# Performance work log

Hardware: AMD Instinct MI355X
Metric: run time of the kernel (lower is better)

The kernel has to match this reference:

```python
import jax, jax.numpy as jnp
import numpy as np

BLOCK_CONFIGS = [[4, 64, 64], [64, 128, 128], [128, 256, 256], [256, 512]]
KNN_K = 16
PN, PL, PM = 5, 3, 3          # kernel polynomial degrees (N, L, M)
BASIS = PN * PL * PM          # 45 monomial basis functions
NUM_LAYERS = 4
N_POINTS = 32768


def get_reduction_schedule(n_input, n_target, num_layers):
    # geometric point-count reduction from n_input down to n_target
    r = (n_target / n_input) ** (1.0 / num_layers)
    return [max(n_target, int(round(n_input * r ** (i + 1)))) for i in range(num_layers)]


def knn_idx(qpos, spos, k):
    # squared distances via the |q|^2 + |s|^2 - 2 q.s identity (avoids (q,s,3) temp)
    d = jnp.sum(qpos * qpos, 1)[:, None] + jnp.sum(spos * spos, 1)[None, :] - 2.0 * (qpos @ spos.T)
    _, idx = jax.lax.top_k(-d, k)  # (q, k) nearest-neighbor indices
    return idx


def poly_basis(r):
    # monomial basis x^i y^j z^k, i<PN, j<PL, k<PM -> (q, k, BASIS)
    x, y, z = r[..., 0], r[..., 1], r[..., 2]
    px = x[..., None] ** jnp.arange(PN)
    py = y[..., None] ** jnp.arange(PL)
    pz = z[..., None] ** jnp.arange(PM)
    phi = px[..., :, None, None] * py[..., None, :, None] * pz[..., None, None, :]
    return phi.reshape(r.shape[:-1] + (BASIS,))


def dcconv(qpos, spos, sfeat, k, W, b, use_pca=True):
    # KNN gather -> normalized relative coords -> (PCA align) -> polynomial kernel conv
    idx = knn_idx(qpos, spos, k)
    r = spos[idx] - qpos[:, None, :]                         # (q, k, 3)
    scale = jnp.max(jnp.sqrt(jnp.sum(r * r, -1)), axis=-1, keepdims=True)
    r = r / (scale[..., None] + 1e-8)
    if use_pca:
        cov = jnp.einsum('qki,qkj->qij', r, r) / k           # (q, 3, 3)
        _, vecs = jnp.linalg.eigh(cov)
        vecs = jax.lax.stop_gradient(vecs)                   # PCA frame treated as constant
        r = jnp.einsum('qki,qij->qkj', r, vecs)
    phi = poly_basis(r)                                       # (q, k, B)
    nf = sfeat[idx]                                           # (q, k, Cin)
    t = jnp.einsum('qkb,qkc->qbc', phi, nf) / k               # neighbor reduce (mean)
    return jnp.einsum('qbc,bco->qo', t, W) + b


def _forward(position_matrix, channel_matrix, ws, bs, ps, head_w, head_b):
    sched = get_reduction_schedule(position_matrix.shape[0], 1, NUM_LAYERS)
    pos, feat = position_matrix, channel_matrix
    li = 0
    for bi, cfg in enumerate(BLOCK_CONFIGS):
        n_sel = sched[bi]
        qpos = pos[:n_sel]                                    # selector: first n_sel centers
        res = feat[:n_sel] @ ps[bi]                           # residual projection
        x, src_pos = feat, pos
        for _ in range(len(cfg) - 1):
            k = min(KNN_K, src_pos.shape[0])
            x = jax.nn.relu(dcconv(qpos, src_pos, x, k, ws[li], bs[li]))
            li += 1
            src_pos = qpos                                    # subsequent layers: self-conv on reduced set
        feat = jax.nn.relu(x + res)
        pos = qpos
    if feat.shape[0] > 1:
        feat = feat.mean(0, keepdims=True)
    return (feat @ head_w + head_b)[0]                        # (out_channels,) = (1,)


def setup_inputs():
    key = jax.random.key(0)
    ks = jax.random.split(key, 32)
    inp = {}
    inp['position_matrix'] = jax.random.normal(ks[0], (N_POINTS, 3), dtype=jnp.float32)
    inp['channel_matrix'] = jax.random.normal(ks[1], (N_POINTS, 4), dtype=jnp.float32)
    i, li = 2, 1
    for cfg in BLOCK_CONFIGS:
        for cin, cout in zip(cfg[:-1], cfg[1:]):
            inp[f'w{li}'] = jax.random.normal(ks[i], (BASIS, cin, cout), dtype=jnp.float32) * 0.05
            inp[f'b{li}'] = jnp.zeros((cout,), dtype=jnp.float32)
            i += 1
            li += 1
    for bi, cfg in enumerate(BLOCK_CONFIGS):
        inp[f'p{bi + 1}'] = jax.random.normal(ks[i], (cfg[0], cfg[-1]), dtype=jnp.float32) * 0.05
        i += 1
    inp['head_w'] = jax.random.normal(ks[i], (BLOCK_CONFIGS[-1][-1], 1), dtype=jnp.float32) * 0.05
    inp['head_b'] = jnp.zeros((1,), dtype=jnp.float32)
    return inp


def reference(position_matrix, channel_matrix, w1, b1, w2, b2, w3, b3, w4, b4, w5, b5, w6, b6, w7, b7,
              p1, p2, p3, p4, head_w, head_b):
    ws = [w1, w2, w3, w4, w5, w6, w7]
    bs = [b1, b2, b3, b4, b5, b6, b7]
    ps = [p1, p2, p3, p4]
    return _forward(position_matrix, channel_matrix, ws, bs, ps, head_w, head_b)
```

## Files before the change

### kernel.cpp

```cpp
#include <hip/hip_runtime.h>
#include <math.h>

#pragma clang fp contract(off)

__device__ __forceinline__ float f_sign(float a, float b) {
    return (b >= 0.0f) ? fabsf(a) : -fabsf(a);
}

__device__ float slapy2(float x, float y) {
    float xa = fabsf(x), ya = fabsf(y);
    float w = fmaxf(xa, ya), z = fminf(xa, ya);
    if (z == 0.0f) return w;
    float t = z / w;
    return w * sqrtf(1.0f + t * t);
}

__device__ void slartg(float f, float g, float &cs, float &sn, float &r) {
    if (g == 0.0f) { cs = 1.0f; sn = 0.0f; r = f; }
    else if (f == 0.0f) { cs = 0.0f; sn = f_sign(1.0f, g); r = fabsf(g); }
    else {
        float d = sqrtf(f * f + g * g);
        float p = 1.0f / d;
        cs = fabsf(f) * p;
        sn = g * f_sign(p, f);
        r = f_sign(d, f);
    }
}

__device__ void slaev2(float a, float b, float c,
                       float &rt1, float &rt2, float &cs1, float &sn1) {
    float sm = a + c, df = a - c, adf = fabsf(df), tb = b + b, ab = fabsf(tb);
    float acmx, acmn;
    if (fabsf(a) > fabsf(c)) { acmx = a; acmn = c; } else { acmx = c; acmn = a; }
    float rt;
    if (adf > ab) { float t = ab / adf; rt = adf * sqrtf(1.0f + t * t); }
    else if (adf < ab) { float t = adf / ab; rt = ab * sqrtf(1.0f + t * t); }
    else rt = ab * sqrtf(2.0f);
    int sgn1;
    if (sm < 0.0f) { rt1 = 0.5f * (sm - rt); sgn1 = -1; rt2 = (acmx / rt1) * acmn - (b / rt1) * b; }
    else if (sm > 0.0f) { rt1 = 0.5f * (sm + rt); sgn1 = 1; rt2 = (acmx / rt1) * acmn - (b / rt1) * b; }
    else { rt1 = 0.5f * rt; rt2 = -0.5f * rt; sgn1 = 1; }
    float cs; int sgn2;
    if (df >= 0.0f) { cs = df + rt; sgn2 = 1; } else { cs = df - rt; sgn2 = -1; }
    float acs = fabsf(cs);
    if (acs > ab) { float ct = -tb / cs; sn1 = 1.0f / sqrtf(1.0f + ct * ct); cs1 = ct * sn1; }
    else {
        if (ab == 0.0f) { cs1 = 1.0f; sn1 = 0.0f; }
        else { float tn = -cs / tb; cs1 = 1.0f / sqrtf(1.0f + tn * tn); sn1 = tn * cs1; }
    }
    if (sgn1 == sgn2) { float tn = cs1; cs1 = -sn1; sn1 = tn; }
}

__device__ void ssteqr3(float *d, float *e, float z[3][3]) {
    const int n = 3;
    const float eps = 5.9604644775390625e-08f;
    const float eps2 = eps * eps;
    const float safmin = 1.1754943508222875e-38f;
    for (int i = 0; i < 3; ++i)
        for (int j = 0; j < 3; ++j)
            z[i][j] = (i == j) ? 1.0f : 0.0f;
    const int nmaxit = n * 30;
    int jtot = 0;
    int l1 = 1;
    int l, m, lend;
    float p, g, r, c, s, f, b, rt1, rt2;
    float wc[2], wsn[2];

L10:
    if (l1 > n) goto L160;
    if (l1 > 1) e[l1 - 2] = 0.0f;
    if (l1 <= n - 1) {
        for (m = l1; m <= n - 1; ++m) {
            float tst = fabsf(e[m - 1]);
            if (tst == 0.0f) goto L30;
            if (tst <= (sqrtf(fabsf(d[m - 1])) * sqrtf(fabsf(d[m]))) * eps) {
                e[m - 1] = 0.0f;
                goto L30;
            }
        }
    }
    m = n;
L30:
    l = l1;
    lend = m;
    l1 = m + 1;
    if (lend == l) goto L10;
    {
        float anorm = 0.0f;
        for (int i = l; i <= lend; ++i) anorm = fmaxf(anorm, fabsf(d[i - 1]));
        for (int i = l; i <= lend - 1; ++i) anorm = fmaxf(anorm, fabsf(e[i - 1]));
        if (anorm == 0.0f) goto L10;
    }
    if (fabsf(d[lend - 1]) < fabsf(d[l - 1])) { int t = lend; lend = l; l = t; }

    if (lend > l) {
L40:
        if (l != lend) {
            bool found = false;
            for (m = l; m <= lend - 1; ++m) {
                float tst = e[m - 1] * e[m - 1];
                if (tst <= (eps2 * fabsf(d[m - 1])) * fabsf(d[m]) + safmin) { found = true; break; }
            }
            if (!found) m = lend;
        } else m = lend;
        if (m < lend) e[m - 1] = 0.0f;
        p = d[l - 1];
        if (m == l) goto L80;
        if (m == l + 1) {
            slaev2(d[l - 1], e[l - 1], d[l], rt1, rt2, c, s);
            for (int i = 0; i < n; ++i) {
                float tmp = z[i][l];
                z[i][l]     = c * tmp - s * z[i][l - 1];
                z[i][l - 1] = s * tmp + c * z[i][l - 1];
            }
            d[l - 1] = rt1; d[l] = rt2; e[l - 1] = 0.0f;
            l += 2;
            if (l <= lend) goto L40;
            goto L140;
        }
        if (jtot == nmaxit) goto L140;
        ++jtot;
        g = (d[l] - p) / (2.0f * e[l - 1]);
        r = slapy2(g, 1.0f);
        g = (d[m - 1] - p) + e[l - 1] / (g + f_sign(r, g));
        s = 1.0f; c = 1.0f; p = 0.0f;
        for (int i = m - 1; i >= l; --i) {
            f = s * e[i - 1];
            b = c * e[i - 1];
            slartg(g, f, c, s, r);
            if (i != m - 1) e[i] = r;
            g = d[i] - p;
            r = (d[i - 1] - g) * s + (2.0f * c) * b;
            p = s * r;
            d[i] = g + p;
            g = c * r - b;
            wc[i - 1] = c;
            wsn[i - 1] = -s;
        }
        for (int jj = m - 1; jj >= l; --jj) {
            float ct = wc[jj - 1], st = wsn[jj - 1];
            for (int i = 0; i < n; ++i) {
                float tmp = z[i][jj];
                z[i][jj]     = ct * tmp - st * z[i][jj - 1];
                z[i][jj - 1] = st * tmp + ct * z[i][jj - 1];
            }
        }
        d[l - 1] -= p;
        e[l - 1] = g;
        goto L40;
L80:
        d[l - 1] = p;
        ++l;
        if (l <= lend) goto L40;
        goto L140;
    } else {
L90:
        if (l != lend) {
            bool found = false;
            for (m = l; m >= lend + 1; --m) {
                float tst = e[m - 2] * e[m - 2];
                if (tst <= (eps2 * fabsf(d[m - 1])) * fabsf(d[m - 2]) + safmin) { found = true; break; }
            }
            if (!found) m = lend;
        } else m = lend;
        if (m > lend) e[m - 2] = 0.0f;
        p = d[l - 1];
        if (m == l) goto L130;
        if (m == l - 1) {
            slaev2(d[l - 2], e[l - 2], d[l - 1], rt1, rt2, c, s);
            for (int i = 0; i < n; ++i) {
                float tmp = z[i][l - 1];
                z[i][l - 1] = c * tmp - s * z[i][l - 2];
                z[i][l - 2] = s * tmp + c * z[i][l - 2];
            }
            d[l - 2] = rt1; d[l - 1] = rt2; e[l - 2] = 0.0f;
            l -= 2;
            if (l >= lend) goto L90;
            goto L140;
        }
        if (jtot == nmaxit) goto L140;
        ++jtot;
        g = (d[l - 2] - p) / (2.0f * e[l - 2]);
        r = slapy2(g, 1.0f);
        g = (d[m - 1] - p) + e[l - 2] / (g + f_sign(r, g));
        s = 1.0f; c = 1.0f; p = 0.0f;
        for (int i = m; i <= l - 1; ++i) {
            f = s * e[i - 1];
            b = c * e[i - 1];
            slartg(g, f, c, s, r);
            if (i != m) e[i - 2] = r;
            g = d[i - 1] - p;
            r = (d[i] - g) * s + (2.0f * c) * b;
            p = s * r;
            d[i - 1] = g + p;
            g = c * r - b;
            wc[i - 1] = c;
            wsn[i - 1] = s;
        }
        for (int jj = m; jj <= l - 1; ++jj) {
            float ct = wc[jj - 1], st = wsn[jj - 1];
            for (int i = 0; i < n; ++i) {
                float tmp = z[i][jj];
                z[i][jj]     = ct * tmp - st * z[i][jj - 1];
                z[i][jj - 1] = st * tmp + ct * z[i][jj - 1];
            }
        }
        d[l - 1] -= p;
        e[l - 2] = g;
        goto L90;
L130:
        d[l - 1] = p;
        --l;
        if (l >= lend) goto L90;
        goto L140;
    }
L140:
    if (jtot < nmaxit) goto L10;
L160:
    for (int ii = 2; ii <= n; ++ii) {
        int i = ii - 1, kk = i;
        float pp = d[i - 1];
        for (int j = ii; j <= n; ++j)
            if (d[j - 1] < pp) { kk = j; pp = d[j - 1]; }
        if (kk != i) {
            d[kk - 1] = d[i - 1];
            d[i - 1] = pp;
            for (int row = 0; row < n; ++row) {
                float t2 = z[row][i - 1];
                z[row][i - 1] = z[row][kk - 1];
                z[row][kk - 1] = t2;
            }
        }
    }
}

__device__ void ssyevd3(float a11, float a21, float a31,
                        float a22, float a32, float a33, float V[3][3]) {
    float tau1, v2, e1;
    float alpha = a21;
    float xnorm = fabsf(a31);
    if (xnorm == 0.0f) {
        tau1 = 0.0f; v2 = 0.0f; e1 = a21;
    } else {
        float beta = -f_sign(slapy2(alpha, xnorm), alpha);
        tau1 = (beta - alpha) / beta;
        float t = 1.0f / (alpha - beta);
        v2 = a31 * t;
        e1 = beta;
        float w1 = tau1 * a22;
        float w2 = tau1 * a32;
        float temp2 = a32 * v2;
        w1 = w1 + tau1 * temp2;
        float temp1 = tau1 * v2;
        w2 = w2 + temp1 * a33;
        float dot = w1;
        dot = dot + w2 * v2;
        float alpha2 = (-0.5f * tau1) * dot;
        w1 = w1 + alpha2;
        w2 = w2 + alpha2 * v2;
        a22 = (a22 - w1) - w1;
        a32 = (a32 - v2 * w1) - w2;
        a33 = (a33 - v2 * w2) - w2 * v2;
    }
    float d[3] = { a11, a22, a33 };
    float e[2] = { e1, a32 };
    float z[3][3];
    ssteqr3(d, e, z);
    for (int j = 0; j < 3; ++j) {
        float wj = z[1][j];
        wj = wj + z[2][j] * v2;
        float temp = (-tau1) * wj;
        V[0][j] = z[0][j];
        V[1][j] = z[1][j] + temp;
        V[2][j] = z[2][j] + v2 * temp;
    }
}

__device__ void geom_body(const float *__restrict__ posf, const int *__restrict__ ord,
                          int q, int k, float *__restrict__ rrot) {
    float qx = posf[3 * q], qy = posf[3 * q + 1], qz = posf[3 * q + 2];
    float rx[16], ry[16], rz[16], nrm[16];
    for (int j = 0; j < k; ++j) {
        int s = ord[j];
        rx[j] = posf[3 * s] - qx;
        ry[j] = posf[3 * s + 1] - qy;
        rz[j] = posf[3 * s + 2] - qz;
        float t = rx[j] * rx[j];
        t = t + ry[j] * ry[j];
        t = t + rz[j] * rz[j];
        nrm[j] = sqrtf(t);
    }
    float scale = nrm[0];
    for (int j = 1; j < k; ++j) scale = fmaxf(scale, nrm[j]);
    float sc = scale + 1e-8f;
    for (int j = 0; j < k; ++j) {
        rx[j] = rx[j] / sc;
        ry[j] = ry[j] / sc;
        rz[j] = rz[j] / sc;
    }
    float c00 = 0.f, c01 = 0.f, c02 = 0.f, c11 = 0.f, c12 = 0.f, c22 = 0.f;
    for (int j = 0; j < k; ++j) {
        c00 = c00 + rx[j] * rx[j];
        c01 = c01 + rx[j] * ry[j];
        c02 = c02 + rx[j] * rz[j];
        c11 = c11 + ry[j] * ry[j];
        c12 = c12 + ry[j] * rz[j];
        c22 = c22 + rz[j] * rz[j];
    }
    float fk = (float)k;
    c00 = c00 / fk; c01 = c01 / fk; c02 = c02 / fk;
    c11 = c11 / fk; c12 = c12 / fk; c22 = c22 / fk;
    float V[3][3];
    ssyevd3(c00, c01, c02, c11, c12, c22, V);
    for (int j = 0; j < k; ++j) {
        for (int col = 0; col < 3; ++col) {
            float a = rx[j] * V[0][col];
            a = a + ry[j] * V[1][col];
            a = a + rz[j] * V[2][col];
            rrot[q * 48 + j * 3 + col] = a;
        }
    }
}


__global__ void prep_kernel(const float *__restrict__ posf, float4 *__restrict__ pos4) {
    int i = blockIdx.x * 256 + threadIdx.x;
    if (i >= 32768) return;
    float x = posf[3 * i], y = posf[3 * i + 1], z = posf[3 * i + 2];
    float t = x * x;
    t = t + y * y;
    t = t + z * z;
    pos4[i] = make_float4(x, y, z, t);
}

__device__ __forceinline__ void insert16(float d, int jbase, int lane,
                                         float &ld, int &li, float &kth) {
    unsigned long long mask = __ballot(d < kth);
    while (mask) {
        int src = __ffsll(mask) - 1;
        mask &= mask - 1;
        float dv = __int_as_float(__builtin_amdgcn_readlane(__float_as_int(d), src));
        int jv = jbase + src;
        if (dv < kth) {
            unsigned long long lm = __ballot((lane < 16) && (ld <= dv));
            int p2 = __popcll(lm);
            float sd = __int_as_float(__builtin_amdgcn_update_dpp(
                0, __float_as_int(ld), 0x111, 0xf, 0xf, true));
            int si = __builtin_amdgcn_update_dpp(0, li, 0x111, 0xf, 0xf, true);
            if (lane < 16) {
                if (lane == p2) { ld = dv; li = jv; }
                else if (lane > p2) { ld = sd; li = si; }
            }
            kth = __int_as_float(__builtin_amdgcn_readlane(__float_as_int(ld), 15));
        }
    }
}

__device__ __forceinline__ void sort64_init(float d, int jbase, int lane,
                                            float &ld, int &li, float &kth) {
    float v = d;
    int vi = jbase + lane;
#pragma unroll
    for (int k2 = 2; k2 <= 64; k2 <<= 1) {
#pragma unroll
        for (int j2 = k2 >> 1; j2 > 0; j2 >>= 1) {
            float ov = __shfl_xor(v, j2);
            int oi = __shfl_xor(vi, j2);
            bool oless = (ov < v) || (ov == v && oi < vi);
            bool dir = ((lane & k2) == 0);
            bool keepmin = (((lane & j2) == 0) == dir);
            bool take = keepmin ? oless : !oless;
            if (take) { v = ov; vi = oi; }
        }
    }
    if (lane < 16) { ld = v; li = vi; }
    kth = __int_as_float(__builtin_amdgcn_readlane(__float_as_int(v), 15));
}

__global__ __launch_bounds__(256) void knng16_kernel(
    const float4 *__restrict__ pos4, const float *__restrict__ posf,
    int S, int *__restrict__ idx_out, float *__restrict__ rrot) {
    __shared__ float md[64];
    __shared__ int mi[64];
    __shared__ int ord[16];
    int q = blockIdx.x;
    int tid = threadIdx.x;
    int lane = tid & 63;
    int w = tid >> 6;
    float4 qp = pos4[q];
    const float FINF = 3.0e38f;
    float ld = FINF;
    int li = 0x7fffffff;
    float kth = FINF;
    int base = w * 256;
    float4 c0, c1, c2, c3;
    bool have = (base + 256 <= S);
    bool first = true;
    if (have) {
        c0 = pos4[base + lane];
        c1 = pos4[base + 64 + lane];
        c2 = pos4[base + 128 + lane];
        c3 = pos4[base + 192 + lane];
    }
    while (have) {
        int nbase = base + 1024;
        bool nhave = (nbase + 256 <= S);
        float4 n0 = c0, n1 = c1, n2 = c2, n3 = c3;
        if (nhave) {
            n0 = pos4[nbase + lane];
            n1 = pos4[nbase + 64 + lane];
            n2 = pos4[nbase + 128 + lane];
            n3 = pos4[nbase + 192 + lane];
        }
        float m0 = fmaf(qp.x, c0.x, 0.0f);
        m0 = fmaf(qp.y, c0.y, m0);
        m0 = fmaf(qp.z, c0.z, m0);
        float d0 = (qp.w + c0.w) - 2.0f * m0;
        float m1 = fmaf(qp.x, c1.x, 0.0f);
        m1 = fmaf(qp.y, c1.y, m1);
        m1 = fmaf(qp.z, c1.z, m1);
        float d1 = (qp.w + c1.w) - 2.0f * m1;
        float m2 = fmaf(qp.x, c2.x, 0.0f);
        m2 = fmaf(qp.y, c2.y, m2);
        m2 = fmaf(qp.z, c2.z, m2);
        float d2 = (qp.w + c2.w) - 2.0f * m2;
        float m3 = fmaf(qp.x, c3.x, 0.0f);
        m3 = fmaf(qp.y, c3.y, m3);
        m3 = fmaf(qp.z, c3.z, m3);
        float d3 = (qp.w + c3.w) - 2.0f * m3;
        if (first) {
            sort64_init(d0, base, lane, ld, li, kth);
            first = false;
        } else {
            insert16(d0, base, lane, ld, li, kth);
        }
        insert16(d1, base + 64, lane, ld, li, kth);
        insert16(d2, base + 128, lane, ld, li, kth);
        insert16(d3, base + 192, lane, ld, li, kth);
        c0 = n0; c1 = n1; c2 = n2; c3 = n3;
        base = nbase;
        have = nhave;
    }
    if (base < S) {
#pragma unroll
        for (int k2 = 0; k2 < 4; ++k2) {
            int j = base + k2 * 64 + lane;
            float dd = FINF;
            if (j < S) {
                float4 p = pos4[j];
                float m = fmaf(qp.x, p.x, 0.0f);
                m = fmaf(qp.y, p.y, m);
                m = fmaf(qp.z, p.z, m);
                dd = (qp.w + p.w) - 2.0f * m;
            }
            insert16(dd, base + k2 * 64, lane, ld, li, kth);
        }
    }
    if (lane < 16) { md[w * 16 + lane] = ld; mi[w * 16 + lane] = li; }
    __syncthreads();
    if (w == 0) {
        int l16 = lane & 15;
        int srcA = (lane >> 5) * 32 + ((lane & 16) ? (16 + (15 - l16)) : l16);
        float v = md[srcA];
        int vi = mi[srcA];
        for (int off = 16; off > 0; off >>= 1) {
            float ov = __shfl_xor(v, off);
            int oi = __shfl_xor(vi, off);
            bool oless = (ov < v) || (ov == v && oi < vi);
            bool take = (lane & off) ? (!oless) : oless;
            if (take) { v = ov; vi = oi; }
        }
        int src2 = (lane < 16) ? lane : (63 - lane);
        float v2 = __shfl(v, src2);
        int vi2 = __shfl(vi, src2);
        for (int off = 16; off > 0; off >>= 1) {
            float ov = __shfl_xor(v2, off);
            int oi = __shfl_xor(vi2, off);
            bool oless = (ov < v2) || (ov == v2 && oi < vi2);
            bool take = (lane & off) ? (!oless) : oless;
            if (take) { v2 = ov; vi2 = oi; }
        }
        if (lane < 16) {
            idx_out[q * 16 + lane] = vi2;
            ord[lane] = vi2;
        }
        if (lane == 0) geom_body(posf, ord, q, 16, rrot);
    }
}

__global__ __launch_bounds__(64) void knngs_kernel(
    const float4 *__restrict__ pos4, const float *__restrict__ posf,
    int S, int k, int *__restrict__ idx_out, float *__restrict__ rrot) {
    __shared__ int ord[16];
    int q = blockIdx.x;
    int lane = threadIdx.x;
    float4 qp = pos4[q];
    const float FINF = 3.0e38f;
    float dist = FINF;
    if (lane < S) {
        float4 p = pos4[lane];
        float m = fmaf(qp.x, p.x, 0.0f);
        m = fmaf(qp.y, p.y, m);
        m = fmaf(qp.z, p.z, m);
        dist = (qp.w + p.w) - 2.0f * m;
    }
    bool used = false;
    for (int r = 0; r < k; ++r) {
        float v = used ? FINF : dist;
        int vid = (used || lane >= S) ? 0x7fffffff : lane;
        for (int off = 32; off > 0; off >>= 1) {
            float ov = __shfl_down(v, off);
            int oid = __shfl_down(vid, off);
            if (ov < v || (ov == v && oid < vid)) { v = ov; vid = oid; }
        }
        vid = __shfl(vid, 0);
        if (lane == 0) { idx_out[q * k + r] = vid; ord[r] = vid; }
        if (lane == vid) used = true;
    }
    if (lane == 0) geom_body(posf, ord, q, k, rrot);
}

__device__ __forceinline__ void compute_phi(const float *rrot, int q, int tid,
                                            double phi[45]) {
    double x = (double)rrot[q * 48 + tid * 3 + 0];
    double y = (double)rrot[q * 48 + tid * 3 + 1];
    double z = (double)rrot[q * 48 + tid * 3 + 2];
    double px[5], py[3], pz[3];
    px[0] = 1.0; px[1] = x; px[2] = x * x; px[3] = px[2] * x; px[4] = px[3] * x;
    py[0] = 1.0; py[1] = y; py[2] = y * y;
    pz[0] = 1.0; pz[1] = z; pz[2] = z * z;
#pragma unroll
    for (int n2 = 0; n2 < 5; ++n2)
#pragma unroll
        for (int l2 = 0; l2 < 3; ++l2)
#pragma unroll
            for (int m2 = 0; m2 < 3; ++m2)
                phi[n2 * 9 + l2 * 3 + m2] = (px[n2] * py[l2]) * pz[m2];
}

__global__ __launch_bounds__(256) void feat_kernel(
    const float *__restrict__ rrot, const int *__restrict__ idx, int k,
    const double *__restrict__ fin64, const float *__restrict__ fin32, int C,
    const float *__restrict__ W, const float *__restrict__ bias, int O,
    double *__restrict__ fout) {
    __shared__ double phi_sh[16][45];
    __shared__ int idx_sh[16];
    __shared__ double red_sh[256];
    extern __shared__ double dyn[];
    double *nf = dyn;
    double *t = dyn + 16 * C;
    int q = blockIdx.x;
    int tid = threadIdx.x;
    int OT = O < 256 ? O : 256;
    int nseg = 256 / OT;
    int o = tid % OT;
    int seg = tid / OT;
    int cseg = C / nseg;
    int c0 = seg * cseg, c1 = c0 + cseg;
    if (tid < k) {
        idx_sh[tid] = idx[q * k + tid];
        double phi[45];
        compute_phi(rrot, q, tid, phi);
#pragma unroll
        for (int b2 = 0; b2 < 45; ++b2) phi_sh[tid][b2] = phi[b2];
    }
    __syncthreads();
    for (int e2 = tid; e2 < k * C; e2 += 256) {
        int j = e2 / C, cc = e2 - j * C;
        size_t src = (size_t)idx_sh[j] * C + cc;
        nf[j * C + cc] = fin32 ? (double)fin32[src] : fin64[src];
    }
    __syncthreads();
    double accp = 0.0;
    for (int ch = 0; ch < 45; ch += 9) {
        for (int e2 = tid; e2 < 9 * C; e2 += 256) {
            int b2 = e2 / C, cc = e2 - b2 * C;
            double a2 = 0.0;
            for (int j = 0; j < k; ++j) a2 = fma(phi_sh[j][ch + b2], nf[j * C + cc], a2);
            t[e2] = a2 / (double)k;
        }
        __syncthreads();
        double a0 = 0.0, a1 = 0.0;
        for (int b2 = 0; b2 < 9; ++b2) {
            const float *wp = W + (size_t)(ch + b2) * C * O + o;
            const double *tp = t + b2 * C;
            int cc = c0;
            for (; cc + 2 <= c1; cc += 2) {
                a0 = fma(tp[cc],     (double)wp[(size_t)cc * O], a0);
                a1 = fma(tp[cc + 1], (double)wp[(size_t)(cc + 1) * O], a1);
            }
            for (; cc < c1; ++cc) a0 = fma(tp[cc], (double)wp[(size_t)cc * O], a0);
        }
        accp += a0 + a1;
        __syncthreads();
    }
    red_sh[tid] = accp;
    __syncthreads();
    if (tid < OT) {
        double v = 0.0;
        for (int s2 = 0; s2 < nseg; ++s2) v += red_sh[tid + s2 * OT];
        v += (double)bias[tid];
        fout[(size_t)q * O + tid] = v > 0.0 ? v : 0.0;
    }
}

__global__ __launch_bounds__(256) void feat64_kernel(
    const float *__restrict__ rrot, const int *__restrict__ idx,
    const double *__restrict__ fin, const float *__restrict__ W,
    const float *__restrict__ bias, int Q, double *__restrict__ fout) {
    __shared__ double phi_sh[2][16][45];
    __shared__ int idx_sh[2][16];
    __shared__ double nf[2][16][64];
    __shared__ double t[2][9][64];
    __shared__ double red[16][64];
    int q0 = blockIdx.x * 2;
    int nq = (Q - q0) < 2 ? (Q - q0) : 2;
    int tid = threadIdx.x;
    int tx = tid & 15;
    int seg = tid >> 4;
    int o0 = tx * 4;
    int cbase = seg * 4;
    if (tid < 32) {
        int qi = tid >> 4, j = tid & 15;
        int qq = q0 + (qi < nq ? qi : 0);
        idx_sh[qi][j] = idx[qq * 16 + j];
        double phi[45];
        compute_phi(rrot, qq, j, phi);
#pragma unroll
        for (int b2 = 0; b2 < 45; ++b2) phi_sh[qi][j][b2] = phi[b2];
    }
    __syncthreads();
    for (int e2 = tid; e2 < 2 * 16 * 64; e2 += 256) {
        int qi = e2 >> 10, j = (e2 >> 6) & 15, cc = e2 & 63;
        nf[qi][j][cc] = fin[(size_t)idx_sh[qi][j] * 64 + cc];
    }
    __syncthreads();
    double acc[2][4] = {{0.0, 0.0, 0.0, 0.0}, {0.0, 0.0, 0.0, 0.0}};
    for (int ch = 0; ch < 45; ch += 9) {
        for (int e2 = tid; e2 < 2 * 9 * 64; e2 += 256) {
            int qi = e2 / 576, rem = e2 - qi * 576;
            int b2 = rem >> 6, cc = rem & 63;
            double a2 = 0.0;
#pragma unroll
            for (int j = 0; j < 16; ++j) a2 = fma(phi_sh[qi][j][ch + b2], nf[qi][j][cc], a2);
            t[qi][b2][cc] = a2 * 0.0625;
        }
        __syncthreads();
#pragma unroll
        for (int b2 = 0; b2 < 9; ++b2) {
            const float *wrow = W + ((size_t)(ch + b2) * 64 + cbase) * 64 + o0;
#pragma unroll
            for (int i = 0; i < 4; ++i) {
                float4 wv = *(const float4 *)(wrow + (size_t)i * 64);
                double w0 = (double)wv.x, w1 = (double)wv.y;
                double w2 = (double)wv.z, w3 = (double)wv.w;
                double tv0 = t[0][b2][cbase + i];
                double tv1 = t[1][b2][cbase + i];
                acc[0][0] = fma(tv0, w0, acc[0][0]);
                acc[0][1] = fma(tv0, w1, acc[0][1]);
                acc[0][2] = fma(tv0, w2, acc[0][2]);
                acc[0][3] = fma(tv0, w3, acc[0][3]);
                acc[1][0] = fma(tv1, w0, acc[1][0]);
                acc[1][1] = fma(tv1, w1, acc[1][1]);
                acc[1][2] = fma(tv1, w2, acc[1][2]);
                acc[1][3] = fma(tv1, w3, acc[1][3]);
            }
        }
        __syncthreads();
    }
    for (int qi = 0; qi < nq; ++qi) {
        red[seg][o0 + 0] = acc[qi][0];
        red[seg][o0 + 1] = acc[qi][1];
        red[seg][o0 + 2] = acc[qi][2];
        red[seg][o0 + 3] = acc[qi][3];
        __syncthreads();
        if (tid < 64) {
            double v = 0.0;
#pragma unroll
            for (int s2 = 0; s2 < 16; ++s2) v += red[s2][tid];
            v += (double)bias[tid];
            fout[(size_t)(q0 + qi) * 64 + tid] = v > 0.0 ? v : 0.0;
        }
        __syncthreads();
    }
}

__global__ __launch_bounds__(256) void t_kernel(
    const float *__restrict__ rrot, const int *__restrict__ idx, int k,
    const double *__restrict__ fin, int C, int q0, double *__restrict__ tbuf,
    double *__restrict__ fout, int O) {
    __shared__ double phi_sh[16][45];
    __shared__ int idx_sh[16];
    extern __shared__ double nf[];
    int q = q0 + blockIdx.x;
    int bch = blockIdx.y * 9;
    int tid = threadIdx.x;
    if (blockIdx.y == 0) {
        for (int i = tid; i < O; i += 256) fout[(size_t)q * O + i] = 0.0;
    }
    if (tid < k) {
        idx_sh[tid] = idx[q * k + tid];
        double phi[45];
        compute_phi(rrot, q, tid, phi);
#pragma unroll
        for (int b2 = 0; b2 < 45; ++b2) phi_sh[tid][b2] = phi[b2];
    }
    __syncthreads();
    for (int e2 = tid; e2 < k * C; e2 += 256) {
        int j = e2 / C, cc = e2 - j * C;
        nf[j * C + cc] = fin[(size_t)idx_sh[j] * C + cc];
    }
    __syncthreads();
    int K = 45 * C;
    for (int e2 = tid; e2 < 9 * C; e2 += 256) {
        int b2 = bch + e2 / C, cc = e2 % C;
        double a2 = 0.0;
        for (int j = 0; j < k; ++j) a2 = fma(phi_sh[j][b2], nf[j * C + cc], a2);
        tbuf[(size_t)blockIdx.x * K + b2 * C + cc] = a2 / (double)k;
    }
}

__global__ __launch_bounds__(256) void gemm_kernel(
    const double *__restrict__ tbuf, const float *__restrict__ W,
    int K, int O, int q0, int q1, int kchunk, double *__restrict__ acc) {
    int OT = O < 256 ? O : 256;
    int qpb = 256 / OT;
    int tid = threadIdx.x;
    int o = blockIdx.x * OT + (tid % OT);
    int q = q0 + blockIdx.y * qpb + tid / OT;
    if (q >= q1) return;
    int k0 = blockIdx.z * kchunk;
    if (k0 >= K) return;
    int kend = min(k0 + kchunk, K);
    const double *tp = tbuf + (size_t)(q - q0) * K;
    const float *wp = W + (size_t)k0 * O + o;
    double a0 = 0.0, a1 = 0.0, a2 = 0.0, a3 = 0.0;
    double a4 = 0.0, a5 = 0.0, a6 = 0.0, a7 = 0.0;
    int kk = k0;
    for (; kk + 8 <= kend; kk += 8) {
        double2 t01 = *(const double2 *)(tp + kk);
        double2 t23 = *(const double2 *)(tp + kk + 2);
        double2 t45 = *(const double2 *)(tp + kk + 4);
        double2 t67 = *(const double2 *)(tp + kk + 6);
        float w0 = wp[0];
        float w1 = wp[(size_t)O];
        float w2 = wp[2 * (size_t)O];
        float w3 = wp[3 * (size_t)O];
        float w4 = wp[4 * (size_t)O];
        float w5 = wp[5 * (size_t)O];
        float w6 = wp[6 * (size_t)O];
        float w7 = wp[7 * (size_t)O];
        a0 = fma(t01.x, (double)w0, a0);
        a1 = fma(t01.y, (double)w1, a1);
        a2 = fma(t23.x, (double)w2, a2);
        a3 = fma(t23.y, (double)w3, a3);
        a4 = fma(t45.x, (double)w4, a4);
        a5 = fma(t45.y, (double)w5, a5);
        a6 = fma(t67.x, (double)w6, a6);
        a7 = fma(t67.y, (double)w7, a7);
        wp += 8 * (size_t)O;
    }
    for (; kk < kend; ++kk) {
        a0 = fma(tp[kk], (double)wp[0], a0);
        wp += (size_t)O;
    }
    double s = ((a0 + a1) + (a2 + a3)) + ((a4 + a5) + (a6 + a7));
    atomicAdd(&acc[(size_t)q * O + o], s);
}

__global__ void finalize_kernel(const float *__restrict__ bias,
                                int Q, int O, double *__restrict__ fout) {
    int i = blockIdx.x * 256 + threadIdx.x;
    if (i >= Q * O) return;
    int o = i % O;
    double v = fout[i] + (double)bias[o];
    fout[i] = v > 0.0 ? v : 0.0;
}

__global__ void resid0_kernel(const float *__restrict__ chanf, const float *__restrict__ p,
                              const double *__restrict__ x, double *__restrict__ fout) {
    int i = blockIdx.x * 256 + threadIdx.x;
    if (i >= 2435 * 64) return;
    int q = i >> 6, o = i & 63;
    const float *f = chanf + 4 * q;
    float c = fmaf(f[0], p[o], 0.0f);
    c = fmaf(f[1], p[64 + o], c);
    c = fmaf(f[2], p[128 + o], c);
    c = fmaf(f[3], p[192 + o], c);
    double v = x[i] + (double)c;
    fout[i] = v > 0.0 ? v : 0.0;
}

__global__ void resid64f_kernel(const float *__restrict__ bias,
                                const double *__restrict__ acc,
                                const double *__restrict__ fin, int Cin,
                                const float *__restrict__ p,
                                int Q, int Cout, double *__restrict__ fout) {
    int i = blockIdx.x * blockDim.x + threadIdx.x;
    if (i >= Q * Cout) return;
    int q = i / Cout, o = i - q * Cout;
    double v = acc[i] + (double)bias[o];
    double x = v > 0.0 ? v : 0.0;
    double a = 0.0;
    for (int c = 0; c < Cin; ++c) a = fma(fin[q * Cin + c], (double)p[c * Cout + o], a);
    double r = x + a;
    fout[i] = r > 0.0 ? r : 0.0;
}

__global__ void head_kernel(const double *__restrict__ feat, const float *__restrict__ hw,
                            const float *__restrict__ hb, float *__restrict__ out) {
    if (threadIdx.x == 0 && blockIdx.x == 0) {
        double acc = 0.0;
        for (int c = 0; c < 512; ++c) acc = fma(feat[c], (double)hw[c], acc);
        out[0] = (float)(acc + (double)hb[0]);
    }
}


extern "C" void kernel_launch(void *const *d_in, const int *in_sizes, int n_in,
                              void *d_out, int out_size, void *d_ws, size_t ws_size,
                              hipStream_t stream) {
    (void)in_sizes; (void)n_in; (void)out_size;

    const float *posf = (const float *)d_in[0];
    const float *chanf = (const float *)d_in[1];
    const float *W[8], *B[8];
    for (int li = 1; li <= 7; ++li) {
        W[li] = (const float *)d_in[2 + 2 * (li - 1)];
        B[li] = (const float *)d_in[3 + 2 * (li - 1)];
    }
    const float *P[5];
    for (int bi = 1; bi <= 4; ++bi) P[bi] = (const float *)d_in[15 + bi];
    const float *hw = (const float *)d_in[20];
    const float *hb = (const float *)d_in[21];

    char *wsb = (char *)d_ws;
    double *B1   = (double *)(wsb + 0);
    double *B2   = (double *)(wsb + 1246720);
    double *B3   = (double *)(wsb + 2493440);
    float *rrot  = (float *)(wsb + 3740160);
    int *idx     = (int *)(wsb + 4207680);
    float4 *pos4 = (float4 *)(wsb + 4363520);
    double *tbuf = (double *)(wsb + 4887808);
    if (ws_size < 9082112) return;

    prep_kernel<<<128, 256, 0, stream>>>(posf, pos4);

    auto knng = [&](int Q, int S, int k) {
        if (S <= 64)
            knngs_kernel<<<Q, 64, 0, stream>>>(pos4, posf, S, k, idx, rrot);
        else
            knng16_kernel<<<Q, 256, 0, stream>>>(pos4, posf, S, idx, rrot);
    };

    auto conv = [&](int Q, int S, int k, const double *fin64, const float *fin32, int C,
                    const float *w, const float *bias, int O, double *fout) {
        knng(Q, S, k);
        size_t dyn = (size_t)(16 + 9) * C * sizeof(double);
        feat_kernel<<<Q, 256, dyn, stream>>>(rrot, idx, k, fin64, fin32, C, w, bias, O, fout);
    };

    auto conv64 = [&](int Q, int S, const double *fin, const float *w,
                      const float *bias, double *fout) {
        knng(Q, S, 16);
        feat64_kernel<<<(Q + 1) / 2, 256, 0, stream>>>(rrot, idx, fin, w, bias, Q, fout);
    };

    auto conv2 = [&](int Q, int S, int k, const double *fin, int C,
                     const float *w, const float *bias, int O, double *fout,
                     int ksplit, bool do_finalize, bool skip_knn) {
        if (!skip_knn) knng(Q, S, k);
        int K = 45 * C;
        int qc = 4194304 / (K * 8);
        if (qc > Q) qc = Q;
        int OT = O < 256 ? O : 256;
        int qpb = 256 / OT;
        int kchunk = (((K + ksplit - 1) / ksplit) + 7) & ~7;
        for (int q0 = 0; q0 < Q; q0 += qc) {
            int qn = min(qc, Q - q0);
            dim3 gt(qn, 5);
            t_kernel<<<gt, 256, (size_t)16 * C * sizeof(double), stream>>>(
                rrot, idx, k, fin, C, q0, tbuf, fout, O);
            dim3 g(O / OT, (qn + qpb - 1) / qpb, ksplit);
            gemm_kernel<<<g, 256, 0, stream>>>(tbuf, w, K, O, q0, q0 + qn, kchunk, fout);
        }
        if (do_finalize)
            finalize_kernel<<<(Q * O + 255) / 256, 256, 0, stream>>>(bias, Q, O, fout);
    };

    conv(2435, 32768, 16, nullptr, chanf, 4, W[1], B[1], 64, B1);
    conv64(2435, 2435, B1, W[2], B[2], B2);
    resid0_kernel<<<(2435 * 64 + 255) / 256, 256, 0, stream>>>(chanf, P[1], B2, B3);
    conv2(181, 2435, 16, B3, 64, W[3], B[3], 128, B1, 24, true, true);
    conv2(181, 181, 16, B1, 128, W[4], B[4], 128, B2, 24, false, false);
    resid64f_kernel<<<(181 * 128 + 255) / 256, 256, 0, stream>>>(
        B[4], B2, B3, 64, P[2], 181, 128, B1);
    conv2(13, 181, 16, B1, 128, W[5], B[5], 256, B2, 96, true, true);
    conv2(13, 13, 13, B2, 256, W[6], B[6], 256, B3, 96, false, false);
    resid64f_kernel<<<(13 * 256 + 255) / 256, 256, 0, stream>>>(
        B[6], B3, B1, 128, P[3], 13, 256, B2);
    conv2(1, 13, 13, B2, 256, W[7], B[7], 512, B1, 256, false, true);
    resid64f_kernel<<<(1 * 512 + 255) / 256, 256, 0, stream>>>(
        B[7], B1, B2, 256, P[4], 1, 512, B3);

    head_kernel<<<1, 64, 0, stream>>>(B3, hw, hb, (float *)d_out);
}
```

Measured before the change: 804.6 us.

## Split large KNN scans across blocks and skip insertion when no candidate beats kth

The KNN scan is factored into a helper. Each 256-candidate chunk now skips the bitonic insert16 work when no lane's minimum distance beats the current 16th-best (checked with a wave ballot). For source sets of 8192 points or more, the scan is split across 4 blocks per query, each writing a partial top-16 to workspace, and a separate merge kernel combines them and runs the geometry step. This adds parallelism for the first layer with many points, at the cost of an extra launch and global traffic for the partial results. The partial buffers reuse the tbuf workspace region.

```diff
diff --git a/kernel.cpp b/kernel.cpp
--- a/kernel.cpp
+++ b/kernel.cpp
@@ -377,24 +377,13 @@
     kth = __int_as_float(__builtin_amdgcn_readlane(__float_as_int(v), 15));
 }
 
-__global__ __launch_bounds__(256) void knng16_kernel(
-    const float4 *__restrict__ pos4, const float *__restrict__ posf,
-    int S, int *__restrict__ idx_out, float *__restrict__ rrot) {
-    __shared__ float md[64];
-    __shared__ int mi[64];
-    __shared__ int ord[16];
-    int q = blockIdx.x;
-    int tid = threadIdx.x;
-    int lane = tid & 63;
-    int w = tid >> 6;
-    float4 qp = pos4[q];
+__device__ __forceinline__ void scan_range(
+    const float4 *__restrict__ pos4, float4 qp, int start, int end, int lane,
+    float &ld, int &li, float &kth) {
     const float FINF = 3.0e38f;
-    float ld = FINF;
-    int li = 0x7fffffff;
-    float kth = FINF;
-    int base = w * 256;
+    int base = start;
     float4 c0, c1, c2, c3;
-    bool have = (base + 256 <= S);
+    bool have = (base + 256 <= end);
     bool first = true;
     if (have) {
         c0 = pos4[base + lane];
@@ -404,7 +393,7 @@
     }
     while (have) {
         int nbase = base + 1024;
-        bool nhave = (nbase + 256 <= S);
+        bool nhave = (nbase + 256 <= end);
         float4 n0 = c0, n1 = c1, n2 = c2, n3 = c3;
         if (nhave) {
             n0 = pos4[nbase + lane];
@@ -428,25 +417,28 @@
         m3 = fmaf(qp.y, c3.y, m3);
         m3 = fmaf(qp.z, c3.z, m3);
         float d3 = (qp.w + c3.w) - 2.0f * m3;
-        if (first) {
-            sort64_init(d0, base, lane, ld, li, kth);
-            first = false;
-        } else {
-            insert16(d0, base, lane, ld, li, kth);
-        }
-        insert16(d1, base + 64, lane, ld, li, kth);
-        insert16(d2, base + 128, lane, ld, li, kth);
-        insert16(d3, base + 192, lane, ld, li, kth);
+        float dmin = fminf(fminf(d0, d1), fminf(d2, d3));
+        if (first || __ballot(dmin < kth)) {
+            if (first) {
+                sort64_init(d0, base, lane, ld, li, kth);
+                first = false;
+            } else {
+                insert16(d0, base, lane, ld, li, kth);
+            }
+            insert16(d1, base + 64, lane, ld, li, kth);
+            insert16(d2, base + 128, lane, ld, li, kth);
+            insert16(d3, base + 192, lane, ld, li, kth);
+        }
         c0 = n0; c1 = n1; c2 = n2; c3 = n3;
         base = nbase;
         have = nhave;
     }
-    if (base < S) {
+    if (base < end) {
 #pragma unroll
         for (int k2 = 0; k2 < 4; ++k2) {
             int j = base + k2 * 64 + lane;
             float dd = FINF;
-            if (j < S) {
+            if (j < end) {
                 float4 p = pos4[j];
                 float m = fmaf(qp.x, p.x, 0.0f);
                 m = fmaf(qp.y, p.y, m);
@@ -456,36 +448,112 @@
             insert16(dd, base + k2 * 64, lane, ld, li, kth);
         }
     }
+}
+
+__device__ __forceinline__ void merge4x16(const float *md, const int *mi,
+                                          int lane, float &v2, int &vi2) {
+    int l16 = lane & 15;
+    int srcA = (lane >> 5) * 32 + ((lane & 16) ? (16 + (15 - l16)) : l16);
+    float v = md[srcA];
+    int vi = mi[srcA];
+    for (int off = 16; off > 0; off >>= 1) {
+        float ov = __shfl_xor(v, off);
+        int oi = __shfl_xor(vi, off);
+        bool oless = (ov < v) || (ov == v && oi < vi);
+        bool take = (lane & off) ? (!oless) : oless;
+        if (take) { v = ov; vi = oi; }
+    }
+    int src2 = (lane < 16) ? lane : (63 - lane);
+    v2 = __shfl(v, src2);
+    vi2 = __shfl(vi, src2);
+    for (int off = 16; off > 0; off >>= 1) {
+        float ov = __shfl_xor(v2, off);
+        int oi = __shfl_xor(vi2, off);
+        bool oless = (ov < v2) || (ov == v2 && oi < vi2);
+        bool take = (lane & off) ? (!oless) : oless;
+        if (take) { v2 = ov; vi2 = oi; }
+    }
+}
+
+__global__ __launch_bounds__(256) void knng16_kernel(
+    const float4 *__restrict__ pos4, const float *__restrict__ posf,
+    int S, int *__restrict__ idx_out, float *__restrict__ rrot) {
+    __shared__ float md[64];
+    __shared__ int mi[64];
+    __shared__ int ord[16];
+    int q = blockIdx.x;
+    int tid = threadIdx.x;
+    int lane = tid & 63;
+    int w = tid >> 6;
+    float4 qp = pos4[q];
+    const float FINF = 3.0e38f;
+    float ld = FINF;
+    int li = 0x7fffffff;
+    float kth = FINF;
+    scan_range(pos4, qp, w * 256, S, lane, ld, li, kth);
     if (lane < 16) { md[w * 16 + lane] = ld; mi[w * 16 + lane] = li; }
     __syncthreads();
     if (w == 0) {
-        int l16 = lane & 15;
-        int srcA = (lane >> 5) * 32 + ((lane & 16) ? (16 + (15 - l16)) : l16);
-        float v = md[srcA];
-        int vi = mi[srcA];
-        for (int off = 16; off > 0; off >>= 1) {
-            float ov = __shfl_xor(v, off);
-            int oi = __shfl_xor(vi, off);
-            bool oless = (ov < v) || (ov == v && oi < vi);
-            bool take = (lane & off) ? (!oless) : oless;
-            if (take) { v = ov; vi = oi; }
-        }
-        int src2 = (lane < 16) ? lane : (63 - lane);
-        float v2 = __shfl(v, src2);
-        int vi2 = __shfl(vi, src2);
-        for (int off = 16; off > 0; off >>= 1) {
-            float ov = __shfl_xor(v2, off);
-            int oi = __shfl_xor(vi2, off);
-            bool oless = (ov < v2) || (ov == v2 && oi < vi2);
-            bool take = (lane & off) ? (!oless) : oless;
-            if (take) { v2 = ov; vi2 = oi; }
-        }
+        float v2; int vi2;
+        merge4x16(md, mi, lane, v2, vi2);
         if (lane < 16) {
             idx_out[q * 16 + lane] = vi2;
             ord[lane] = vi2;
         }
         if (lane == 0) geom_body(posf, ord, q, 16, rrot);
     }
+}
+
+
+__global__ __launch_bounds__(256) void knn_scan_kernel(
+    const float4 *__restrict__ pos4, int S, int span,
+    float *__restrict__ md_g, int *__restrict__ mi_g) {
+    __shared__ float md[64];
+    __shared__ int mi[64];
+    int b = blockIdx.x;
+    int q = blockIdx.y;
+    int nblk = gridDim.x;
+    int tid = threadIdx.x;
+    int lane = tid & 63;
+    int w = tid >> 6;
+    float4 qp = pos4[q];
+    const float FINF = 3.0e38f;
+    float ld = FINF;
+    int li = 0x7fffffff;
+    float kth = FINF;
+    int start = b * span;
+    int end = min(S, start + span);
+    scan_range(pos4, qp, start + w * 256, end, lane, ld, li, kth);
+    if (lane < 16) { md[w * 16 + lane] = ld; mi[w * 16 + lane] = li; }
+    __syncthreads();
+    if (w == 0) {
+        float v2; int vi2;
+        merge4x16(md, mi, lane, v2, vi2);
+        if (lane < 16) {
+            md_g[((size_t)q * nblk + b) * 16 + lane] = v2;
+            mi_g[((size_t)q * nblk + b) * 16 + lane] = vi2;
+        }
+    }
+}
+
+__global__ __launch_bounds__(64) void knn_merge_kernel(
+    const float *__restrict__ md_g, const int *__restrict__ mi_g,
+    const float *__restrict__ posf, int *__restrict__ idx_out,
+    float *__restrict__ rrot) {
+    __shared__ float md[64];
+    __shared__ int mi[64];
+    __shared__ int ord[16];
+    int q = blockIdx.x;
+    int lane = threadIdx.x;
+    md[lane] = md_g[(size_t)q * 64 + lane];
+    mi[lane] = mi_g[(size_t)q * 64 + lane];
+    float v2; int vi2;
+    merge4x16(md, mi, lane, v2, vi2);
+    if (lane < 16) {
+        idx_out[q * 16 + lane] = vi2;
+        ord[lane] = vi2;
+    }
+    if (lane == 0) geom_body(posf, ord, q, 16, rrot);
 }
 
 __global__ __launch_bounds__(64) void knngs_kernel(
@@ -842,15 +910,24 @@
     int *idx     = (int *)(wsb + 4207680);
     float4 *pos4 = (float4 *)(wsb + 4363520);
     double *tbuf = (double *)(wsb + 4887808);
+    float *md_g  = (float *)(wsb + 4887808);
+    int *mi_g    = (int *)(wsb + 4887808 + 623360);
     if (ws_size < 9082112) return;
 
     prep_kernel<<<128, 256, 0, stream>>>(posf, pos4);
 
     auto knng = [&](int Q, int S, int k) {
-        if (S <= 64)
+        if (S <= 64) {
             knngs_kernel<<<Q, 64, 0, stream>>>(pos4, posf, S, k, idx, rrot);
-        else
+        } else if (S >= 8192) {
+            const int nblk = 4;
+            int span = ((S + nblk - 1) / nblk + 1023) & ~1023;
+            dim3 g(nblk, Q);
+            knn_scan_kernel<<<g, 256, 0, stream>>>(pos4, S, span, md_g, mi_g);
+            knn_merge_kernel<<<Q, 64, 0, stream>>>(md_g, mi_g, posf, idx, rrot);
+        } else {
             knng16_kernel<<<Q, 256, 0, stream>>>(pos4, posf, S, idx, rrot);
+        }
     };
 
     auto conv = [&](int Q, int S, int k, const double *fin64, const float *fin32, int C,
```

Result: slower. 907.5 us (+12.8%).

## Split geometry into its own parallel kernel and skip KNN insert when no candidate qualifies

Applied to the files above, without the earlier changes.

Moves the per-query geometry (covariance, eigen-decomposition, rotation) out of the KNN kernels, where a single lane ran it serially at the end of each block, into a separate kernel that gives each query its own thread. It also adds a wave-wide early-out in the KNN scan: when none of the four distances per lane beats the current k-th best, all insert16 calls for that chunk are skipped. The cost is an extra kernel launch per layer and a round trip of the indices through global memory before the geometry step.

```diff
diff --git a/kernel.cpp b/kernel.cpp
--- a/kernel.cpp
+++ b/kernel.cpp
@@ -322,6 +322,14 @@
     }
 }
 
+__global__ __launch_bounds__(256) void geom_kernel(
+    const float *__restrict__ posf, const int *__restrict__ idx,
+    int Q, int k, float *__restrict__ rrot) {
+    int q = blockIdx.x * 256 + threadIdx.x;
+    if (q >= Q) return;
+    geom_body(posf, idx + (size_t)q * k, q, k, rrot);
+}
+
 
 __global__ void prep_kernel(const float *__restrict__ posf, float4 *__restrict__ pos4) {
     int i = blockIdx.x * 256 + threadIdx.x;
@@ -377,24 +385,13 @@
     kth = __int_as_float(__builtin_amdgcn_readlane(__float_as_int(v), 15));
 }
 
-__global__ __launch_bounds__(256) void knng16_kernel(
-    const float4 *__restrict__ pos4, const float *__restrict__ posf,
-    int S, int *__restrict__ idx_out, float *__restrict__ rrot) {
-    __shared__ float md[64];
-    __shared__ int mi[64];
-    __shared__ int ord[16];
-    int q = blockIdx.x;
-    int tid = threadIdx.x;
-    int lane = tid & 63;
-    int w = tid >> 6;
-    float4 qp = pos4[q];
+__device__ __forceinline__ void scan_range(
+    const float4 *__restrict__ pos4, float4 qp, int start, int end, int lane,
+    float &ld, int &li, float &kth) {
     const float FINF = 3.0e38f;
-    float ld = FINF;
-    int li = 0x7fffffff;
-    float kth = FINF;
-    int base = w * 256;
+    int base = start;
     float4 c0, c1, c2, c3;
-    bool have = (base + 256 <= S);
+    bool have = (base + 256 <= end);
     bool first = true;
     if (have) {
         c0 = pos4[base + lane];
@@ -404,7 +401,7 @@
     }
     while (have) {
         int nbase = base + 1024;
-        bool nhave = (nbase + 256 <= S);
+        bool nhave = (nbase + 256 <= end);
         float4 n0 = c0, n1 = c1, n2 = c2, n3 = c3;
         if (nhave) {
             n0 = pos4[nbase + lane];
@@ -428,25 +425,28 @@
         m3 = fmaf(qp.y, c3.y, m3);
         m3 = fmaf(qp.z, c3.z, m3);
         float d3 = (qp.w + c3.w) - 2.0f * m3;
-        if (first) {
-            sort64_init(d0, base, lane, ld, li, kth);
-            first = false;
-        } else {
-            insert16(d0, base, lane, ld, li, kth);
-        }
-        insert16(d1, base + 64, lane, ld, li, kth);
-        insert16(d2, base + 128, lane, ld, li, kth);
-        insert16(d3, base + 192, lane, ld, li, kth);
+        float dmin = fminf(fminf(d0, d1), fminf(d2, d3));
+        if (first || __ballot(dmin < kth)) {
+            if (first) {
+                sort64_init(d0, base, lane, ld, li, kth);
+                first = false;
+            } else {
+                insert16(d0, base, lane, ld, li, kth);
+            }
+            insert16(d1, base + 64, lane, ld, li, kth);
+            insert16(d2, base + 128, lane, ld, li, kth);
+            insert16(d3, base + 192, lane, ld, li, kth);
+        }
         c0 = n0; c1 = n1; c2 = n2; c3 = n3;
         base = nbase;
         have = nhave;
     }
-    if (base < S) {
+    if (base < end) {
 #pragma unroll
         for (int k2 = 0; k2 < 4; ++k2) {
             int j = base + k2 * 64 + lane;
             float dd = FINF;
-            if (j < S) {
+            if (j < end) {
                 float4 p = pos4[j];
                 float m = fmaf(qp.x, p.x, 0.0f);
                 m = fmaf(qp.y, p.y, m);
@@ -456,42 +456,58 @@
             insert16(dd, base + k2 * 64, lane, ld, li, kth);
         }
     }
+}
+
+__device__ __forceinline__ void merge4x16(const float *md, const int *mi,
+                                          int lane, float &v2, int &vi2) {
+    int l16 = lane & 15;
+    int srcA = (lane >> 5) * 32 + ((lane & 16) ? (16 + (15 - l16)) : l16);
+    float v = md[srcA];
+    int vi = mi[srcA];
+    for (int off = 16; off > 0; off >>= 1) {
+        float ov = __shfl_xor(v, off);
+        int oi = __shfl_xor(vi, off);
+        bool oless = (ov < v) || (ov == v && oi < vi);
+        bool take = (lane & off) ? (!oless) : oless;
+        if (take) { v = ov; vi = oi; }
+    }
+    int src2 = (lane < 16) ? lane : (63 - lane);
+    v2 = __shfl(v, src2);
+    vi2 = __shfl(vi, src2);
+    for (int off = 16; off > 0; off >>= 1) {
+        float ov = __shfl_xor(v2, off);
+        int oi = __shfl_xor(vi2, off);
+        bool oless = (ov < v2) || (ov == v2 && oi < vi2);
+        bool take = (lane & off) ? (!oless) : oless;
+        if (take) { v2 = ov; vi2 = oi; }
+    }
+}
+
+__global__ __launch_bounds__(256) void knng16_kernel(
+    const float4 *__restrict__ pos4, int S, int *__restrict__ idx_out) {
+    __shared__ float md[64];
+    __shared__ int mi[64];
+    int q = blockIdx.x;
+    int tid = threadIdx.x;
+    int lane = tid & 63;
+    int w = tid >> 6;
+    float4 qp = pos4[q];
+    const float FINF = 3.0e38f;
+    float ld = FINF;
+    int li = 0x7fffffff;
+    float kth = FINF;
+    scan_range(pos4, qp, w * 256, S, lane, ld, li, kth);
     if (lane < 16) { md[w * 16 + lane] = ld; mi[w * 16 + lane] = li; }
     __syncthreads();
     if (w == 0) {
-        int l16 = lane & 15;
-        int srcA = (lane >> 5) * 32 + ((lane & 16) ? (16 + (15 - l16)) : l16);
-        float v = md[srcA];
-        int vi = mi[srcA];
-        for (int off = 16; off > 0; off >>= 1) {
-            float ov = __shfl_xor(v, off);
-            int oi = __shfl_xor(vi, off);
-            bool oless = (ov < v) || (ov == v && oi < vi);
-            bool take = (lane & off) ? (!oless) : oless;
-            if (take) { v = ov; vi = oi; }
-        }
-        int src2 = (lane < 16) ? lane : (63 - lane);
-        float v2 = __shfl(v, src2);
-        int vi2 = __shfl(vi, src2);
-        for (int off = 16; off > 0; off >>= 1) {
-            float ov = __shfl_xor(v2, off);
-            int oi = __shfl_xor(vi2, off);
-            bool oless = (ov < v2) || (ov == v2 && oi < vi2);
-            bool take = (lane & off) ? (!oless) : oless;
-            if (take) { v2 = ov; vi2 = oi; }
-        }
-        if (lane < 16) {
-            idx_out[q * 16 + lane] = vi2;
-            ord[lane] = vi2;
-        }
-        if (lane == 0) geom_body(posf, ord, q, 16, rrot);
+        float v2; int vi2;
+        merge4x16(md, mi, lane, v2, vi2);
+        if (lane < 16) idx_out[q * 16 + lane] = vi2;
     }
 }
 
 __global__ __launch_bounds__(64) void knngs_kernel(
-    const float4 *__restrict__ pos4, const float *__restrict__ posf,
-    int S, int k, int *__restrict__ idx_out, float *__restrict__ rrot) {
-    __shared__ int ord[16];
+    const float4 *__restrict__ pos4, int S, int k, int *__restrict__ idx_out) {
     int q = blockIdx.x;
     int lane = threadIdx.x;
     float4 qp = pos4[q];
@@ -514,10 +530,9 @@
             if (ov < v || (ov == v && oid < vid)) { v = ov; vid = oid; }
         }
         vid = __shfl(vid, 0);
-        if (lane == 0) { idx_out[q * k + r] = vid; ord[r] = vid; }
+        if (lane == 0) idx_out[q * k + r] = vid;
         if (lane == vid) used = true;
     }
-    if (lane == 0) geom_body(posf, ord, q, k, rrot);
 }
 
 __device__ __forceinline__ void compute_phi(const float *rrot, int q, int tid,
@@ -848,9 +863,10 @@
 
     auto knng = [&](int Q, int S, int k) {
         if (S <= 64)
-            knngs_kernel<<<Q, 64, 0, stream>>>(pos4, posf, S, k, idx, rrot);
+            knngs_kernel<<<Q, 64, 0, stream>>>(pos4, S, k, idx);
         else
-            knng16_kernel<<<Q, 256, 0, stream>>>(pos4, posf, S, idx, rrot);
+            knng16_kernel<<<Q, 256, 0, stream>>>(pos4, S, idx);
+        geom_kernel<<<(Q + 255) / 256, 256, 0, stream>>>(posf, idx, Q, k, rrot);
     };
 
     auto conv = [&](int Q, int S, int k, const double *fin64, const float *fin32, int C,
```

Measured after the change: 790.8 us. About the same (-1.7%).
